# Kernel optimization log

Hardware: AMD Instinct MI355X
Metric: run time of the kernel (lower is better)

## Reference

```python
import jax, jax.numpy as jnp
import numpy as np

N_HEADS = 8
TOP_K = 2
EPS = 1e-5


def cross_node(x4, nf, tkv, Wq, bq, Wk, bk, Wv, bv, Wo, bo, gamma, beta, token_mask):
    # x4: [N, BL, 1, D]; nf: [N, BL, K, D]; tkv: [N, K, 1]; token_mask: [N] float (routed subset)
    N, BL, _, D = x4.shape
    K = nf.shape[2]
    H = N_HEADS
    dh = D // H
    nf = nf * tkv[:, None, :, :]  # use_weights: scale neighbors by topk similarity weights
    xf = x4.reshape(N * BL, D)
    nff = nf.reshape(N * BL, K, D)
    q = (xf @ Wq.T + bq).reshape(N * BL, H, dh)
    k = (nff @ Wk.T + bk).reshape(N * BL, K, H, dh)
    v = (nff @ Wv.T + bv).reshape(N * BL, K, H, dh)
    # flash_attn_func math: scaled dot-product over the K neighbors, per head
    scores = jnp.einsum('thd,tkhd->thk', q, k) / jnp.sqrt(jnp.asarray(dh, xf.dtype))
    attn = jax.nn.softmax(scores, axis=-1)
    o = jnp.einsum('thk,tkhd->thd', attn, v).reshape(N * BL, D)
    o = o @ Wo.T + bo
    # masked BatchNorm1d (training-mode batch stats over ONLY the gathered/routed tokens,
    # matching torch where each expert sees just its subset)
    m = jnp.broadcast_to(token_mask[:, None], (N, BL)).reshape(-1, 1)
    cnt = jnp.maximum(m.sum(), 1.0)
    mean = (o * m).sum(0) / cnt
    var = (((o - mean) ** 2) * m).sum(0) / cnt
    o = (o - mean) / jnp.sqrt(var + EPS) * gamma + beta
    return (o + xf).reshape(N, BL, D)


def moe_forward(x, mm, topk_values, Wr, br, eWq, eWk, eWv, eWo, ebq, ebk, ebv, ebo,
                eGamma, eBeta, eW1, eb1, mWq, mWk, mWv, mWo, mbq, mbk, mbv, mbo,
                mGamma, mBeta, mW2, mb2, topk_indices, modality_index):
    N, B, L, D = x.shape
    BL = B * L
    K = topk_indices.shape[1]
    E = Wr.shape[0]
    Mn = mWq.shape[0]
    # neighbor gather: nf[n, b*l, k] = x[topk_indices[n, k], b, l]
    nf = jnp.transpose(x[topk_indices], (0, 2, 3, 1, 4)).reshape(N, BL, K, D)
    x4 = x.reshape(N, BL, 1, D)
    tkv = topk_values.reshape(N, K, 1)
    # router softmax gating
    gate = jax.nn.softmax(mm.reshape(N, D) @ Wr.T + br, axis=-1)  # [N, E]
    _, te = jax.lax.top_k(gate, TOP_K)
    routed = jax.nn.one_hot(te, E, dtype=gate.dtype).sum(1)  # [N, E] 0/1
    f_i = routed.sum(0) / N
    P_i = gate.sum(0) / N
    balance_loss = E * jnp.sum(f_i * P_i)
    # capacity limiting via running cumsum per expert column
    keep = jnp.cumsum(routed, axis=0) <= (N / E)
    rprobs = gate * jnp.where(keep, routed, jnp.zeros_like(routed))
    active = rprobs.sum(-1) > 0  # [N]
    eprobs, eidx = jax.lax.top_k(rprobs, TOP_K)  # [N, TOP_K]
    # expert dispatch/combine (dense-masked equivalent of the per-expert gather/scatter)
    out_tok = jnp.zeros((N, BL, D), x.dtype)
    for i in range(E):
        sel = (eidx == i).any(-1) & active  # tokens gathered for expert i
        mask_f = sel.astype(x.dtype)
        prob_i = (eprobs * (eidx == i)).sum(-1)  # combine weight (0 for capacity-dropped)
        co = cross_node(x4, nf, tkv, eWq[i], ebq[i], eWk[i], ebk[i], eWv[i], ebv[i],
                        eWo[i], ebo[i], eGamma[i], eBeta[i], mask_f)
        co = co @ eW1[i].T + eb1[i]
        out_tok = out_tok + (mask_f * prob_i)[:, None, None] * co
    # modality experts: every token with modality m goes through modality expert m
    mod_out = jnp.zeros_like(out_tok)
    for m in range(Mn):
        mask_f = (modality_index[:, m, :] == 1).any(-1).astype(x.dtype)
        co = cross_node(x4, nf, tkv, mWq[m], mbq[m], mWk[m], mbk[m], mWv[m], mbv[m],
                        mWo[m], mbo[m], mGamma[m], mBeta[m], mask_f)
        co = co @ mW2[m].T + mb2[m]
        mod_out = mod_out + mask_f[:, None, None] * co
    out = (out_tok + mod_out / Mn).reshape(N, B, L, D)
    return out, balance_loss


def setup_inputs():
    key = jax.random.key(0)
    ks = jax.random.split(key, 7)
    N, B, L, D, K, E, Mn = 1024, 2, 8, 128, 16, 4, 4
    s = 1.0 / float(np.sqrt(D))
    inp = {}
    inp['x'] = jax.random.normal(ks[0], (N, B, L, D), jnp.float32)
    inp['mm'] = jax.random.normal(ks[1], (N, 1, D), jnp.float32)
    inp['topk_values'] = jax.random.uniform(ks[2], (N, K), jnp.float32)
    inp['topk_indices'] = jax.random.randint(ks[3], (N, K), 0, N, dtype=jnp.int32)
    inp['modality_index'] = jax.nn.one_hot(
        jax.random.randint(ks[4], (N,), 0, Mn, dtype=jnp.int32), Mn, dtype=jnp.int32
    ).reshape(N, Mn, 1)
    inp['Wr'] = jax.random.normal(ks[5], (E, D), jnp.float32) * s
    inp['br'] = jnp.zeros((E,), jnp.float32)
    kk = jax.random.split(ks[6], 10)
    for j, nm in enumerate(['eWq', 'eWk', 'eWv', 'eWo', 'eW1']):
        inp[nm] = jax.random.normal(kk[j], (E, D, D), jnp.float32) * s
    for j, nm in enumerate(['mWq', 'mWk', 'mWv', 'mWo', 'mW2']):
        inp[nm] = jax.random.normal(kk[5 + j], (Mn, D, D), jnp.float32) * s
    for nm in ['ebq', 'ebk', 'ebv', 'ebo', 'eBeta', 'eb1']:
        inp[nm] = jnp.zeros((E, D), jnp.float32)
    for nm in ['mbq', 'mbk', 'mbv', 'mbo', 'mBeta', 'mb2']:
        inp[nm] = jnp.zeros((Mn, D), jnp.float32)
    inp['eGamma'] = jnp.ones((E, D), jnp.float32)
    inp['mGamma'] = jnp.ones((Mn, D), jnp.float32)
    return inp


def reference(x, mm, topk_values, topk_indices, modality_index, Wr, br,
              eWq, eWk, eWv, eWo, ebq, ebk, ebv, ebo, eGamma, eBeta, eW1, eb1,
              mWq, mWk, mWv, mWo, mbq, mbk, mbv, mbo, mGamma, mBeta, mW2, mb2):
    return moe_forward(x, mm, topk_values, Wr, br, eWq, eWk, eWv, eWo, ebq, ebk, ebv, ebo,
                       eGamma, eBeta, eW1, eb1, mWq, mWk, mWv, mWo, mbq, mbk, mbv, mbo,
                       mGamma, mBeta, mW2, mb2, topk_indices, modality_index)
```

## Files before the change

### kernel.cpp

```cpp
#include <hip/hip_runtime.h>

typedef unsigned short u16;
typedef unsigned int u32;
typedef short short8 __attribute__((ext_vector_type(8)));
typedef float f32x4 __attribute__((ext_vector_type(4)));

#define NTOK 1024
#define TT 16384
#define DD 128
#define EPSV 1e-5f
#define ST 2097152

__device__ __forceinline__ u16 f2bf(float f) {
    u32 u = __float_as_uint(f);
    u += 0x7fffu + ((u >> 16) & 1u);
    return (u16)(u >> 16);
}
__device__ __forceinline__ u32 pack2(u16 a, u16 b) { return (u32)a | ((u32)b << 16); }
__device__ __forceinline__ void up2(u32 w, float& lo, float& hi) {
    lo = __uint_as_float(w << 16);
    hi = __uint_as_float(w & 0xffff0000u);
}

__global__ __launch_bounds__(256) void k_prep(const float* __restrict__ x,
        const float* __restrict__ eWq, const float* __restrict__ eWk,
        const float* __restrict__ eWv, const float* __restrict__ eWo, const float* __restrict__ eW1,
        const float* __restrict__ mWq, const float* __restrict__ mWk, const float* __restrict__ mWv,
        const float* __restrict__ mWo, const float* __restrict__ mW2,
        const float* __restrict__ mm, const float* __restrict__ Wr, const float* __restrict__ br,
        u16* __restrict__ Xb, u16* __restrict__ Wb, float* __restrict__ logits) {
    int bid = blockIdx.x; int tid = threadIdx.x;
    if (bid < 1024) {
        int i = bid * 256 + tid;
        const float4* p = (const float4*)x + (size_t)i * 2;
        float4 a = p[0], b = p[1];
        uint4 o;
        o.x = pack2(f2bf(a.x), f2bf(a.y));
        o.y = pack2(f2bf(a.z), f2bf(a.w));
        o.z = pack2(f2bf(b.x), f2bf(b.y));
        o.w = pack2(f2bf(b.z), f2bf(b.w));
        *((uint4*)Xb + i) = o;
    } else if (bid < 1344) {
        int i = (bid - 1024) * 256 + tid;
        int tns = i >> 13;
        int off = (i & 8191) * 8;
        const float* src;
        switch (tns) {
            case 0: src = eWq; break; case 1: src = eWk; break; case 2: src = eWv; break;
            case 3: src = eWo; break; case 4: src = eW1; break; case 5: src = mWq; break;
            case 6: src = mWk; break; case 7: src = mWv; break; case 8: src = mWo; break;
            default: src = mW2; break;
        }
        const float4* p = (const float4*)(src + off);
        float4 a = p[0], b = p[1];
        uint4 o;
        o.x = pack2(f2bf(a.x), f2bf(a.y));
        o.y = pack2(f2bf(a.z), f2bf(a.w));
        o.z = pack2(f2bf(b.x), f2bf(b.y));
        o.w = pack2(f2bf(b.z), f2bf(b.w));
        *(uint4*)(Wb + tns * 65536 + off) = o;
    } else {
        int i = (bid - 1344) * 256 + tid;
        int n = i >> 2, e = i & 3;
        const float4* a = (const float4*)(mm + (size_t)n * DD);
        const float4* w = (const float4*)(Wr + (size_t)e * DD);
        float s = 0.f;
#pragma unroll
        for (int j = 0; j < 32; j++) {
            float4 av = a[j], wv = w[j];
            s += av.x * wv.x + av.y * wv.y + av.z * wv.z + av.w * wv.w;
        }
        logits[i] = s + br[e];
    }
}

__global__ __launch_bounds__(1024) void k_route(const float* __restrict__ logits, const int* __restrict__ modix,
                                                float* __restrict__ mask8, float* __restrict__ comb8,
                                                float* __restrict__ cnt8, float* __restrict__ bnsum,
                                                float* __restrict__ bnsq, float* __restrict__ loss) {
    __shared__ int wsum[4][16];
    __shared__ float red[16];
    int n = threadIdx.x;
    if (n < 16) red[n] = 0.f;
    bnsum[n] = 0.f; bnsq[n] = 0.f;
    float g[4];
    float mx = -1e30f;
#pragma unroll
    for (int e = 0; e < 4; e++) { g[e] = logits[n * 4 + e]; mx = fmaxf(mx, g[e]); }
    float s = 0.f;
#pragma unroll
    for (int e = 0; e < 4; e++) { g[e] = expf(g[e] - mx); s += g[e]; }
    float inv = 1.f / s;
#pragma unroll
    for (int e = 0; e < 4; e++) g[e] *= inv;
    int i0 = 0; float b0 = g[0];
#pragma unroll
    for (int e = 1; e < 4; e++) if (g[e] > b0) { b0 = g[e]; i0 = e; }
    int i1 = -1; float b1v = -1e30f;
#pragma unroll
    for (int e = 0; e < 4; e++) if (e != i0 && g[e] > b1v) { b1v = g[e]; i1 = e; }
    u32 rbits = (1u << i0) | (1u << i1);
    int wav = n >> 6, lane = n & 63;
    unsigned long long lm = (~0ull) >> (63 - lane);
    int pre[4];
#pragma unroll
    for (int e = 0; e < 4; e++) {
        unsigned long long m = __ballot((rbits >> e) & 1u);
        pre[e] = __popcll(m & lm);
        if (lane == 63) wsum[e][wav] = __popcll(m);
    }
    __syncthreads();
    float rp[4]; float rsum = 0.f;
#pragma unroll
    for (int e = 0; e < 4; e++) {
        int off = 0;
        for (int w = 0; w < 16; w++) if (w < wav) off += wsum[e][w];
        bool keep = (off + pre[e]) <= 256;
        rp[e] = (((rbits >> e) & 1u) && keep) ? g[e] : 0.f;
        rsum += rp[e];
    }
    bool active = rsum > 0.f;
    int j0 = 0; float c0 = rp[0];
#pragma unroll
    for (int e = 1; e < 4; e++) if (rp[e] > c0) { c0 = rp[e]; j0 = e; }
    int j1 = -1; float c1 = -1e30f;
#pragma unroll
    for (int e = 0; e < 4; e++) if (e != j0 && rp[e] > c1) { c1 = rp[e]; j1 = e; }
    float vals[16];
#pragma unroll
    for (int e = 0; e < 4; e++) {
        bool sel = active && (e == j0 || e == j1);
        float mf = sel ? 1.f : 0.f;
        mask8[e * NTOK + n] = mf;
        comb8[e * NTOK + n] = rp[e];
        vals[e] = mf;
    }
#pragma unroll
    for (int m = 0; m < 4; m++) {
        float mf = (modix[n * 4 + m] == 1) ? 1.f : 0.f;
        mask8[(4 + m) * NTOK + n] = mf;
        comb8[(4 + m) * NTOK + n] = 0.25f * mf;
        vals[4 + m] = mf;
    }
#pragma unroll
    for (int e = 0; e < 4; e++) vals[8 + e] = ((rbits >> e) & 1u) ? 1.f : 0.f;
#pragma unroll
    for (int e = 0; e < 4; e++) vals[12 + e] = g[e];
#pragma unroll
    for (int q = 0; q < 16; q++) {
        float v = vals[q];
        for (int off = 32; off; off >>= 1) v += __shfl_down(v, off, 64);
        if (lane == 0) atomicAdd(&red[q], v);
    }
    __syncthreads();
    if (n == 0) {
        for (int c = 0; c < 8; c++) cnt8[c] = fmaxf(16.f * red[c], 1.f);
        float l = 0.f;
        for (int e = 0; e < 4; e++) l += (red[8 + e] / 1024.f) * (red[12 + e] / 1024.f);
        loss[0] = 4.f * l;
    }
}

__global__ __launch_bounds__(256) void k_gemm_qkv(const u16* __restrict__ Xb, const u16* __restrict__ Wb,
        const float* __restrict__ ebq, const float* __restrict__ mbq,
        const float* __restrict__ mask8,
        u16* __restrict__ Qb, u16* __restrict__ Kb, u16* __restrict__ Vb) {
    __shared__ u16 As[64 * 128];
    __shared__ u16 Bs[128 * 128];
    int tid = threadIdx.x; int bm = blockIdx.x; int c = blockIdx.y;
    int wq = (c < 4) ? c : 20 + (c - 4);
    int wk = (c < 4) ? 4 + c : 24 + (c - 4);
    int wv = (c < 4) ? 8 + c : 28 + (c - 4);
    const u16* Wsl[3] = { Wb + wq * 16384, Wb + wk * 16384, Wb + wv * 16384 };
    const float* bq = (c < 4) ? (ebq + c * 128) : (mbq + (c - 4) * 128);
    u16* Os[3] = { Qb + (size_t)c * ST, Kb + (size_t)c * ST, Vb + (size_t)c * ST };
    const float* maskp = mask8 + c * NTOK;
    bool qact = (maskp[bm * 4] != 0.f) || (maskp[bm * 4 + 1] != 0.f) ||
                (maskp[bm * 4 + 2] != 0.f) || (maskp[bm * 4 + 3] != 0.f);

    const uint4* asrc = (const uint4*)(Xb + (size_t)bm * 8192);
#pragma unroll
    for (int it = 0; it < 4; ++it) {
        int ci = it * 256 + tid;
        uint4 v = asrc[ci];
        int byte = ci * 16; int row = byte >> 8;
        *(uint4*)((char*)As + (byte ^ ((row & 7) << 4))) = v;
    }
    __syncthreads();
    int lane = tid & 63, wid = tid >> 6, lr = lane & 15, lg = lane >> 4;
    short8 a[4];
#pragma unroll
    for (int ks = 0; ks < 4; ++ks) {
        int kk = ks * 64 + lg * 16;
        int arow = wid * 16 + lr;
        a[ks] = *(const short8*)((const char*)As + ((arow * 256 + kk) ^ ((arow & 7) << 4)));
    }
    for (int y = 0; y < 3; ++y) {
        if (y == 0 && !qact) continue;
        const uint4* wsrc = (const uint4*)Wsl[y];
#pragma unroll
        for (int it = 0; it < 8; ++it) {
            int qi = it * 256 + tid;
            uint4 v = wsrc[qi];
            int eo = qi * 8; int row = eo >> 7; int byte = eo * 2;
            *(uint4*)((char*)Bs + (byte ^ ((row & 7) << 4))) = v;
        }
        __syncthreads();
        f32x4 acc[8] = {};
#pragma unroll
        for (int ks = 0; ks < 4; ++ks) {
            int kk = ks * 64 + lg * 16;
#pragma unroll
            for (int nc = 0; nc < 8; ++nc) {
                int brow = nc * 16 + lr;
                short8 b = *(const short8*)((const char*)Bs + ((brow * 256 + kk) ^ ((brow & 7) << 4)));
                acc[nc] = __builtin_amdgcn_mfma_f32_16x16x32_bf16(a[ks], b, acc[nc], 0, 0, 0);
            }
        }
        int row0 = bm * 64 + wid * 16 + lg * 4;
        u16* Op = Os[y];
        bool hasb = (y == 0);
#pragma unroll
        for (int nc = 0; nc < 8; ++nc) {
            int col = nc * 16 + lr;
            float bb = hasb ? bq[col] : 0.f;
#pragma unroll
            for (int r = 0; r < 4; r++)
                Op[(size_t)(row0 + r) * 128 + col] = f2bf(acc[nc][r] + bb);
        }
        __syncthreads();
    }
}

__global__ __launch_bounds__(256) void k_attn(const u16* Qb, const u16* __restrict__ Kb,
        const u16* __restrict__ Vb, const float* __restrict__ tkv, const int* __restrict__ idx,
        const float* __restrict__ ebk, const float* __restrict__ ebv,
        const float* __restrict__ mbk, const float* __restrict__ mbv,
        const float* __restrict__ mask8, u16* Ob) {
    int bid = blockIdx.x;
    int c = bid & 7, inner = bid >> 3;
    int tid = threadIdx.x;
    int gid = inner * 256 + tid;
    int t = gid >> 3, h = gid & 7;
    int n = __builtin_amdgcn_readfirstlane(t >> 4);
    int bl = t & 15;
    if (mask8[c * NTOK + n] == 0.f) return;
    const u16* Qc = Qb + (size_t)c * ST;
    const u16* Kc = Kb + (size_t)c * ST;
    const u16* Vc = Vb + (size_t)c * ST;
    u16* Oc = Ob + (size_t)c * ST;
    const float* bk = (c < 4) ? (ebk + c * 128) : (mbk + (c - 4) * 128);
    const float* bv = (c < 4) ? (ebv + c * 128) : (mbv + (c - 4) * 128);
    float qv[16];
    {
        const uint4* qp = (const uint4*)(Qc + (size_t)t * 128 + h * 16);
        uint4 a = qp[0], b = qp[1];
        up2(a.x, qv[0], qv[1]);   up2(a.y, qv[2], qv[3]);
        up2(a.z, qv[4], qv[5]);   up2(a.w, qv[6], qv[7]);
        up2(b.x, qv[8], qv[9]);   up2(b.y, qv[10], qv[11]);
        up2(b.z, qv[12], qv[13]); up2(b.w, qv[14], qv[15]);
    }
    float qb = 0.f;
#pragma unroll
    for (int i = 0; i < 16; i++) qb += qv[i] * bk[h * 16 + i];
    int gsav[16]; float tsav[16];
#pragma unroll
    for (int k = 0; k < 16; k++) { gsav[k] = idx[n * 16 + k]; tsav[k] = tkv[n * 16 + k]; }
    float scv[16]; float smax = -1e30f;
#pragma unroll 2
    for (int k = 0; k < 16; k++) {
        const uint4* kp = (const uint4*)(Kc + (size_t)(gsav[k] * 16 + bl) * 128 + h * 16);
        uint4 a = kp[0], b = kp[1];
        float d0 = 0.f, d1 = 0.f, lo, hi;
        up2(a.x, lo, hi); d0 = fmaf(lo, qv[0], d0);  d1 = fmaf(hi, qv[1], d1);
        up2(a.y, lo, hi); d0 = fmaf(lo, qv[2], d0);  d1 = fmaf(hi, qv[3], d1);
        up2(a.z, lo, hi); d0 = fmaf(lo, qv[4], d0);  d1 = fmaf(hi, qv[5], d1);
        up2(a.w, lo, hi); d0 = fmaf(lo, qv[6], d0);  d1 = fmaf(hi, qv[7], d1);
        up2(b.x, lo, hi); d0 = fmaf(lo, qv[8], d0);  d1 = fmaf(hi, qv[9], d1);
        up2(b.y, lo, hi); d0 = fmaf(lo, qv[10], d0); d1 = fmaf(hi, qv[11], d1);
        up2(b.z, lo, hi); d0 = fmaf(lo, qv[12], d0); d1 = fmaf(hi, qv[13], d1);
        up2(b.w, lo, hi); d0 = fmaf(lo, qv[14], d0); d1 = fmaf(hi, qv[15], d1);
        float sv = 0.25f * (tsav[k] * (d0 + d1) + qb);
        scv[k] = sv; smax = fmaxf(smax, sv);
    }
    float sum = 0.f;
#pragma unroll
    for (int k = 0; k < 16; k++) { scv[k] = expf(scv[k] - smax); sum += scv[k]; }
    float inv = 1.f / sum;
    float o[16];
#pragma unroll
    for (int i = 0; i < 16; i++) o[i] = 0.f;
#pragma unroll 2
    for (int k = 0; k < 16; k++) {
        const uint4* vp = (const uint4*)(Vc + (size_t)(gsav[k] * 16 + bl) * 128 + h * 16);
        uint4 a = vp[0], b = vp[1];
        float cc = scv[k] * inv * tsav[k];
        float lo, hi;
        up2(a.x, lo, hi); o[0] = fmaf(lo, cc, o[0]);   o[1] = fmaf(hi, cc, o[1]);
        up2(a.y, lo, hi); o[2] = fmaf(lo, cc, o[2]);   o[3] = fmaf(hi, cc, o[3]);
        up2(a.z, lo, hi); o[4] = fmaf(lo, cc, o[4]);   o[5] = fmaf(hi, cc, o[5]);
        up2(a.w, lo, hi); o[6] = fmaf(lo, cc, o[6]);   o[7] = fmaf(hi, cc, o[7]);
        up2(b.x, lo, hi); o[8] = fmaf(lo, cc, o[8]);   o[9] = fmaf(hi, cc, o[9]);
        up2(b.y, lo, hi); o[10] = fmaf(lo, cc, o[10]); o[11] = fmaf(hi, cc, o[11]);
        up2(b.z, lo, hi); o[12] = fmaf(lo, cc, o[12]); o[13] = fmaf(hi, cc, o[13]);
        up2(b.w, lo, hi); o[14] = fmaf(lo, cc, o[14]); o[15] = fmaf(hi, cc, o[15]);
    }
#pragma unroll
    for (int i = 0; i < 16; i++) o[i] += bv[h * 16 + i];
    uint4 s0, s1;
    s0.x = pack2(f2bf(o[0]), f2bf(o[1]));  s0.y = pack2(f2bf(o[2]), f2bf(o[3]));
    s0.z = pack2(f2bf(o[4]), f2bf(o[5]));  s0.w = pack2(f2bf(o[6]), f2bf(o[7]));
    s1.x = pack2(f2bf(o[8]), f2bf(o[9]));  s1.y = pack2(f2bf(o[10]), f2bf(o[11]));
    s1.z = pack2(f2bf(o[12]), f2bf(o[13])); s1.w = pack2(f2bf(o[14]), f2bf(o[15]));
    uint4* op = (uint4*)(Oc + (size_t)t * 128 + h * 16);
    op[0] = s0; op[1] = s1;
}

__global__ __launch_bounds__(256) void k_gemm_o(const u16* __restrict__ Ab, const u16* __restrict__ Wb,
        const float* __restrict__ ebo, const float* __restrict__ mbo,
        u16* __restrict__ O2, const float* __restrict__ mask8,
        float* __restrict__ bnsum, float* __restrict__ bnsq) {
    __shared__ u16 As[64 * 128];
    __shared__ u16 Bs[128 * 128];
    __shared__ float ssum[128], ssq[128];
    int tid = threadIdx.x; int bm = blockIdx.x; int c = blockIdx.y;
    const float* maskp = mask8 + c * NTOK;
    if (maskp[bm * 4] == 0.f && maskp[bm * 4 + 1] == 0.f &&
        maskp[bm * 4 + 2] == 0.f && maskp[bm * 4 + 3] == 0.f) return;
    int wo = (c < 4) ? 12 + c : 32 + (c - 4);
    const u16* Wp = Wb + wo * 16384;
    const float* bo = (c < 4) ? (ebo + c * 128) : (mbo + (c - 4) * 128);
    if (tid < 128) { ssum[tid] = 0.f; ssq[tid] = 0.f; }
    const uint4* asrc = (const uint4*)(Ab + (size_t)c * ST + (size_t)bm * 8192);
#pragma unroll
    for (int it = 0; it < 4; ++it) {
        int ci = it * 256 + tid;
        uint4 v = asrc[ci];
        int byte = ci * 16; int row = byte >> 8;
        *(uint4*)((char*)As + (byte ^ ((row & 7) << 4))) = v;
    }
    const uint4* wsrc = (const uint4*)Wp;
#pragma unroll
    for (int it = 0; it < 8; ++it) {
        int qi = it * 256 + tid;
        uint4 v = wsrc[qi];
        int eo = qi * 8; int row = eo >> 7; int byte = eo * 2;
        *(uint4*)((char*)Bs + (byte ^ ((row & 7) << 4))) = v;
    }
    __syncthreads();
    int lane = tid & 63, wid = tid >> 6, lr = lane & 15, lg = lane >> 4;
    f32x4 acc[8] = {};
#pragma unroll
    for (int ks = 0; ks < 4; ++ks) {
        int kk = ks * 64 + lg * 16;
        int arow = wid * 16 + lr;
        short8 a = *(const short8*)((const char*)As + ((arow * 256 + kk) ^ ((arow & 7) << 4)));
#pragma unroll
        for (int nc = 0; nc < 8; ++nc) {
            int brow = nc * 16 + lr;
            short8 b = *(const short8*)((const char*)Bs + ((brow * 256 + kk) ^ ((brow & 7) << 4)));
            acc[nc] = __builtin_amdgcn_mfma_f32_16x16x32_bf16(a, b, acc[nc], 0, 0, 0);
        }
    }
    int nidx = bm * 4 + wid;
    float mk = maskp[nidx];
    int row0 = bm * 64 + wid * 16 + lg * 4;
    u16* O2c = O2 + (size_t)c * ST;
    float ps[8], pq[8];
#pragma unroll
    for (int nc = 0; nc < 8; ++nc) {
        int col = nc * 16 + lr;
        float bb = bo[col];
        float sv = 0.f, qv = 0.f;
#pragma unroll
        for (int r = 0; r < 4; r++) {
            float v = acc[nc][r] + bb;
            if (mk != 0.f) O2c[(size_t)(row0 + r) * 128 + col] = f2bf(v);
            sv += v; qv += v * v;
        }
        ps[nc] = sv * mk; pq[nc] = qv * mk;
    }
#pragma unroll
    for (int nc = 0; nc < 8; ++nc) {
        ps[nc] += __shfl_xor(ps[nc], 16, 64); ps[nc] += __shfl_xor(ps[nc], 32, 64);
        pq[nc] += __shfl_xor(pq[nc], 16, 64); pq[nc] += __shfl_xor(pq[nc], 32, 64);
    }
    if (lane < 16) {
#pragma unroll
        for (int nc = 0; nc < 8; ++nc) {
            atomicAdd(&ssum[nc * 16 + lane], ps[nc]);
            atomicAdd(&ssq[nc * 16 + lane], pq[nc]);
        }
    }
    __syncthreads();
    if (tid < 128) { atomicAdd(&bnsum[c * 128 + tid], ssum[tid]); atomicAdd(&bnsq[c * 128 + tid], ssq[tid]); }
}

__global__ __launch_bounds__(512) void k_gemm_w1(const u16* __restrict__ O2, const u16* __restrict__ Xb,
        const u16* __restrict__ Wb, const float* __restrict__ eb1, const float* __restrict__ mb2,
        const float* __restrict__ eGamma, const float* __restrict__ mGamma,
        const float* __restrict__ eBeta, const float* __restrict__ mBeta,
        const float* __restrict__ comb8, const float* __restrict__ cnt8,
        const float* __restrict__ bnsum, const float* __restrict__ bnsq,
        float* __restrict__ out) {
    __shared__ u16 As[64 * 128];
    __shared__ u16 Bs[128 * 128];
    __shared__ float scall[8][128], shall[8][128];
    int tid = threadIdx.x; int bm = blockIdx.x;
#pragma unroll
    for (int j = 0; j < 2; ++j) {
        int id = j * 512 + tid;
        int c = id >> 7, d = id & 127;
        float cnt = cnt8[c];
        float mean = bnsum[c * 128 + d] / cnt;
        float var = bnsq[c * 128 + d] / cnt - mean * mean;
        float rs = rsqrtf(var + EPSV);
        const float* ga = (c < 4) ? (eGamma + c * 128) : (mGamma + (c - 4) * 128);
        const float* be = (c < 4) ? (eBeta + c * 128) : (mBeta + (c - 4) * 128);
        float gg = ga[d];
        scall[c][d] = rs * gg;
        shall[c][d] = be[d] - mean * rs * gg;
    }
    __syncthreads();
    int lane = tid & 63, wid = tid >> 6, lr = lane & 15, lg = lane >> 4;
    int wm = wid & 3, wn = wid >> 2;
    f32x4 acc[4] = {};
    const uint4* xsrc = (const uint4*)(Xb + (size_t)bm * 8192);
    for (int c = 0; c < 8; ++c) {
        float wc4[4];
        wc4[0] = comb8[c * NTOK + bm * 4];     wc4[1] = comb8[c * NTOK + bm * 4 + 1];
        wc4[2] = comb8[c * NTOK + bm * 4 + 2]; wc4[3] = comb8[c * NTOK + bm * 4 + 3];
        if (wc4[0] == 0.f && wc4[1] == 0.f && wc4[2] == 0.f && wc4[3] == 0.f) continue;
        int wsl = (c < 4) ? 16 + c : 36 + (c - 4);
        const u16* Wp = Wb + wsl * 16384;
        const uint4* osrc = (const uint4*)(O2 + (size_t)c * ST + (size_t)bm * 8192);
#pragma unroll
        for (int it = 0; it < 2; ++it) {
            int qi = it * 512 + tid;
            int eo = qi * 8; int row = eo >> 7; int cb = eo & 127;
            float wc = wc4[row >> 4];
            uint4 ov = osrc[qi]; uint4 xv = xsrc[qi];
            float olo, ohi, xlo, xhi;
            uint4 hh;
            up2(ov.x, olo, ohi); up2(xv.x, xlo, xhi);
            hh.x = pack2(f2bf((olo * scall[c][cb] + shall[c][cb] + xlo) * wc),
                         f2bf((ohi * scall[c][cb + 1] + shall[c][cb + 1] + xhi) * wc));
            up2(ov.y, olo, ohi); up2(xv.y, xlo, xhi);
            hh.y = pack2(f2bf((olo * scall[c][cb + 2] + shall[c][cb + 2] + xlo) * wc),
                         f2bf((ohi * scall[c][cb + 3] + shall[c][cb + 3] + xhi) * wc));
            up2(ov.z, olo, ohi); up2(xv.z, xlo, xhi);
            hh.z = pack2(f2bf((olo * scall[c][cb + 4] + shall[c][cb + 4] + xlo) * wc),
                         f2bf((ohi * scall[c][cb + 5] + shall[c][cb + 5] + xhi) * wc));
            up2(ov.w, olo, ohi); up2(xv.w, xlo, xhi);
            hh.w = pack2(f2bf((olo * scall[c][cb + 6] + shall[c][cb + 6] + xlo) * wc),
                         f2bf((ohi * scall[c][cb + 7] + shall[c][cb + 7] + xhi) * wc));
            *(uint4*)((char*)As + ((eo * 2) ^ ((row & 7) << 4))) = hh;
        }
        const uint4* wsrc = (const uint4*)Wp;
#pragma unroll
        for (int it = 0; it < 4; ++it) {
            int qi = it * 512 + tid;
            uint4 v = wsrc[qi];
            int eo = qi * 8; int row = eo >> 7; int byte = eo * 2;
            *(uint4*)((char*)Bs + (byte ^ ((row & 7) << 4))) = v;
        }
        __syncthreads();
#pragma unroll
        for (int ks = 0; ks < 4; ++ks) {
            int kk = ks * 64 + lg * 16;
            int arow = wm * 16 + lr;
            short8 a = *(const short8*)((const char*)As + ((arow * 256 + kk) ^ ((arow & 7) << 4)));
#pragma unroll
            for (int nc = 0; nc < 4; ++nc) {
                int brow = wn * 64 + nc * 16 + lr;
                short8 b = *(const short8*)((const char*)Bs + ((brow * 256 + kk) ^ ((brow & 7) << 4)));
                acc[nc] = __builtin_amdgcn_mfma_f32_16x16x32_bf16(a, b, acc[nc], 0, 0, 0);
            }
        }
        __syncthreads();
    }
    int nidx = bm * 4 + wm;
    int row0 = bm * 64 + wm * 16 + lg * 4;
    float wc8[8];
#pragma unroll
    for (int c = 0; c < 8; ++c) wc8[c] = comb8[c * NTOK + nidx];
#pragma unroll
    for (int nc = 0; nc < 4; ++nc) {
        int col = wn * 64 + nc * 16 + lr;
        float bias = 0.f;
#pragma unroll
        for (int c = 0; c < 8; ++c) {
            const float* b1 = (c < 4) ? (eb1 + c * 128) : (mb2 + (c - 4) * 128);
            bias += wc8[c] * b1[col];
        }
#pragma unroll
        for (int r = 0; r < 4; r++)
            out[(size_t)(row0 + r) * 128 + col] = acc[nc][r] + bias;
    }
}

extern "C" void kernel_launch(void* const* d_in, const int* in_sizes, int n_in,
                              void* d_out, int out_size, void* d_ws, size_t ws_size,
                              hipStream_t stream) {
    (void)in_sizes; (void)n_in; (void)ws_size; (void)out_size;
    const float* x    = (const float*)d_in[0];
    const float* mm   = (const float*)d_in[1];
    const float* tkv  = (const float*)d_in[2];
    const int*   idx  = (const int*)d_in[3];
    const int*   modi = (const int*)d_in[4];
    const float* Wr   = (const float*)d_in[5];
    const float* br   = (const float*)d_in[6];
    const float* eWq = (const float*)d_in[7],  *eWk = (const float*)d_in[8],  *eWv = (const float*)d_in[9];
    const float* eWo = (const float*)d_in[10], *eW1 = (const float*)d_in[11];
    const float* mWq = (const float*)d_in[12], *mWk = (const float*)d_in[13], *mWv = (const float*)d_in[14];
    const float* mWo = (const float*)d_in[15], *mW2 = (const float*)d_in[16];
    const float* ebq = (const float*)d_in[17], *ebk = (const float*)d_in[18], *ebv = (const float*)d_in[19];
    const float* ebo = (const float*)d_in[20], *eBeta = (const float*)d_in[21], *eb1 = (const float*)d_in[22];
    const float* mbq = (const float*)d_in[23], *mbk = (const float*)d_in[24], *mbv = (const float*)d_in[25];
    const float* mbo = (const float*)d_in[26], *mBeta = (const float*)d_in[27], *mb2 = (const float*)d_in[28];
    const float* eGamma = (const float*)d_in[29], *mGamma = (const float*)d_in[30];
    float* out = (float*)d_out;

    char* wsb = (char*)d_ws;
    const size_t MB = 1024 * 1024;
    u16* Xb = (u16*)wsb;
    u16* Wb = (u16*)(wsb + 4 * MB);
    u16* Qb = (u16*)(wsb + 8 * MB);
    u16* Kb = (u16*)(wsb + 40 * MB);
    u16* Vb = (u16*)(wsb + 72 * MB);
    u16* O2 = (u16*)(wsb + 104 * MB);
    float* logits = (float*)(wsb + 136 * MB);
    float* comb8 = logits + 4096;
    float* mask8 = comb8 + 8192;
    float* cnt8  = mask8 + 8192;
    float* bnsum = cnt8 + 16;
    float* bnsq  = bnsum + 1024;

    k_prep<<<1360, 256, 0, stream>>>(x, eWq, eWk, eWv, eWo, eW1, mWq, mWk, mWv, mWo, mW2,
                                     mm, Wr, br, Xb, Wb, logits);
    k_route<<<1, 1024, 0, stream>>>(logits, modi, mask8, comb8, cnt8, bnsum, bnsq,
                                    out + (size_t)TT * DD);
    k_gemm_qkv<<<dim3(256, 8), 256, 0, stream>>>(Xb, Wb, ebq, mbq, mask8, Qb, Kb, Vb);
    k_attn<<<4096, 256, 0, stream>>>(Qb, Kb, Vb, tkv, idx, ebk, ebv, mbk, mbv, mask8, Qb);
    k_gemm_o<<<dim3(256, 8), 256, 0, stream>>>(Qb, Wb, ebo, mbo, O2, mask8, bnsum, bnsq);
    k_gemm_w1<<<256, 512, 0, stream>>>(O2, Xb, Wb, eb1, mb2, eGamma, mGamma, eBeta, mBeta,
                                       comb8, cnt8, bnsum, bnsq, out);
}
```

Measured before the change: 119.0 us.

## Fuse neighbor attention into output-projection GEMM via shared-memory A tile

```diff
diff --git a/kernel.cpp b/kernel.cpp
--- a/kernel.cpp
+++ b/kernel.cpp
@@ -20,6 +20,9 @@
 __device__ __forceinline__ void up2(u32 w, float& lo, float& hi) {
     lo = __uint_as_float(w << 16);
     hi = __uint_as_float(w & 0xffff0000u);
+}
+__device__ __forceinline__ float rfl_f(float v) {
+    return __uint_as_float(__builtin_amdgcn_readfirstlane(__float_as_uint(v)));
 }
 
 __global__ __launch_bounds__(256) void k_prep(const float* __restrict__ x,
@@ -232,144 +235,146 @@
     }
 }
 
-__global__ __launch_bounds__(256) void k_attn(const u16* Qb, const u16* __restrict__ Kb,
+__global__ __launch_bounds__(512) void k_attn_o(const u16* __restrict__ Qb, const u16* __restrict__ Kb,
         const u16* __restrict__ Vb, const float* __restrict__ tkv, const int* __restrict__ idx,
         const float* __restrict__ ebk, const float* __restrict__ ebv,
         const float* __restrict__ mbk, const float* __restrict__ mbv,
-        const float* __restrict__ mask8, u16* Ob) {
-    int bid = blockIdx.x;
-    int c = bid & 7, inner = bid >> 3;
-    int tid = threadIdx.x;
-    int gid = inner * 256 + tid;
-    int t = gid >> 3, h = gid & 7;
-    int n = __builtin_amdgcn_readfirstlane(t >> 4);
-    int bl = t & 15;
-    if (mask8[c * NTOK + n] == 0.f) return;
-    const u16* Qc = Qb + (size_t)c * ST;
-    const u16* Kc = Kb + (size_t)c * ST;
-    const u16* Vc = Vb + (size_t)c * ST;
-    u16* Oc = Ob + (size_t)c * ST;
-    const float* bk = (c < 4) ? (ebk + c * 128) : (mbk + (c - 4) * 128);
-    const float* bv = (c < 4) ? (ebv + c * 128) : (mbv + (c - 4) * 128);
-    float qv[16];
-    {
-        const uint4* qp = (const uint4*)(Qc + (size_t)t * 128 + h * 16);
-        uint4 a = qp[0], b = qp[1];
-        up2(a.x, qv[0], qv[1]);   up2(a.y, qv[2], qv[3]);
-        up2(a.z, qv[4], qv[5]);   up2(a.w, qv[6], qv[7]);
-        up2(b.x, qv[8], qv[9]);   up2(b.y, qv[10], qv[11]);
-        up2(b.z, qv[12], qv[13]); up2(b.w, qv[14], qv[15]);
-    }
-    float qb = 0.f;
-#pragma unroll
-    for (int i = 0; i < 16; i++) qb += qv[i] * bk[h * 16 + i];
-    int gsav[16]; float tsav[16];
-#pragma unroll
-    for (int k = 0; k < 16; k++) { gsav[k] = idx[n * 16 + k]; tsav[k] = tkv[n * 16 + k]; }
-    float scv[16]; float smax = -1e30f;
-#pragma unroll 2
-    for (int k = 0; k < 16; k++) {
-        const uint4* kp = (const uint4*)(Kc + (size_t)(gsav[k] * 16 + bl) * 128 + h * 16);
-        uint4 a = kp[0], b = kp[1];
-        float d0 = 0.f, d1 = 0.f, lo, hi;
-        up2(a.x, lo, hi); d0 = fmaf(lo, qv[0], d0);  d1 = fmaf(hi, qv[1], d1);
-        up2(a.y, lo, hi); d0 = fmaf(lo, qv[2], d0);  d1 = fmaf(hi, qv[3], d1);
-        up2(a.z, lo, hi); d0 = fmaf(lo, qv[4], d0);  d1 = fmaf(hi, qv[5], d1);
-        up2(a.w, lo, hi); d0 = fmaf(lo, qv[6], d0);  d1 = fmaf(hi, qv[7], d1);
-        up2(b.x, lo, hi); d0 = fmaf(lo, qv[8], d0);  d1 = fmaf(hi, qv[9], d1);
-        up2(b.y, lo, hi); d0 = fmaf(lo, qv[10], d0); d1 = fmaf(hi, qv[11], d1);
-        up2(b.z, lo, hi); d0 = fmaf(lo, qv[12], d0); d1 = fmaf(hi, qv[13], d1);
-        up2(b.w, lo, hi); d0 = fmaf(lo, qv[14], d0); d1 = fmaf(hi, qv[15], d1);
-        float sv = 0.25f * (tsav[k] * (d0 + d1) + qb);
-        scv[k] = sv; smax = fmaxf(smax, sv);
-    }
-    float sum = 0.f;
-#pragma unroll
-    for (int k = 0; k < 16; k++) { scv[k] = expf(scv[k] - smax); sum += scv[k]; }
-    float inv = 1.f / sum;
-    float o[16];
-#pragma unroll
-    for (int i = 0; i < 16; i++) o[i] = 0.f;
-#pragma unroll 2
-    for (int k = 0; k < 16; k++) {
-        const uint4* vp = (const uint4*)(Vc + (size_t)(gsav[k] * 16 + bl) * 128 + h * 16);
-        uint4 a = vp[0], b = vp[1];
-        float cc = scv[k] * inv * tsav[k];
-        float lo, hi;
-        up2(a.x, lo, hi); o[0] = fmaf(lo, cc, o[0]);   o[1] = fmaf(hi, cc, o[1]);
-        up2(a.y, lo, hi); o[2] = fmaf(lo, cc, o[2]);   o[3] = fmaf(hi, cc, o[3]);
-        up2(a.z, lo, hi); o[4] = fmaf(lo, cc, o[4]);   o[5] = fmaf(hi, cc, o[5]);
-        up2(a.w, lo, hi); o[6] = fmaf(lo, cc, o[6]);   o[7] = fmaf(hi, cc, o[7]);
-        up2(b.x, lo, hi); o[8] = fmaf(lo, cc, o[8]);   o[9] = fmaf(hi, cc, o[9]);
-        up2(b.y, lo, hi); o[10] = fmaf(lo, cc, o[10]); o[11] = fmaf(hi, cc, o[11]);
-        up2(b.z, lo, hi); o[12] = fmaf(lo, cc, o[12]); o[13] = fmaf(hi, cc, o[13]);
-        up2(b.w, lo, hi); o[14] = fmaf(lo, cc, o[14]); o[15] = fmaf(hi, cc, o[15]);
-    }
-#pragma unroll
-    for (int i = 0; i < 16; i++) o[i] += bv[h * 16 + i];
-    uint4 s0, s1;
-    s0.x = pack2(f2bf(o[0]), f2bf(o[1]));  s0.y = pack2(f2bf(o[2]), f2bf(o[3]));
-    s0.z = pack2(f2bf(o[4]), f2bf(o[5]));  s0.w = pack2(f2bf(o[6]), f2bf(o[7]));
-    s1.x = pack2(f2bf(o[8]), f2bf(o[9]));  s1.y = pack2(f2bf(o[10]), f2bf(o[11]));
-    s1.z = pack2(f2bf(o[12]), f2bf(o[13])); s1.w = pack2(f2bf(o[14]), f2bf(o[15]));
-    uint4* op = (uint4*)(Oc + (size_t)t * 128 + h * 16);
-    op[0] = s0; op[1] = s1;
-}
-
-__global__ __launch_bounds__(256) void k_gemm_o(const u16* __restrict__ Ab, const u16* __restrict__ Wb,
-        const float* __restrict__ ebo, const float* __restrict__ mbo,
-        u16* __restrict__ O2, const float* __restrict__ mask8,
+        const u16* __restrict__ Wb, const float* __restrict__ ebo, const float* __restrict__ mbo,
+        const float* __restrict__ mask8, u16* __restrict__ O2,
         float* __restrict__ bnsum, float* __restrict__ bnsq) {
     __shared__ u16 As[64 * 128];
     __shared__ u16 Bs[128 * 128];
     __shared__ float ssum[128], ssq[128];
-    int tid = threadIdx.x; int bm = blockIdx.x; int c = blockIdx.y;
+    int bid = blockIdx.x;
+    int c = bid & 7, bm = bid >> 3;
     const float* maskp = mask8 + c * NTOK;
-    if (maskp[bm * 4] == 0.f && maskp[bm * 4 + 1] == 0.f &&
-        maskp[bm * 4 + 2] == 0.f && maskp[bm * 4 + 3] == 0.f) return;
+    float m4[4];
+    m4[0] = maskp[bm * 4];     m4[1] = maskp[bm * 4 + 1];
+    m4[2] = maskp[bm * 4 + 2]; m4[3] = maskp[bm * 4 + 3];
+    if (m4[0] == 0.f && m4[1] == 0.f && m4[2] == 0.f && m4[3] == 0.f) return;
+    int tid = threadIdx.x;
+    if (tid < 128) { ssum[tid] = 0.f; ssq[tid] = 0.f; }
     int wo = (c < 4) ? 12 + c : 32 + (c - 4);
-    const u16* Wp = Wb + wo * 16384;
-    const float* bo = (c < 4) ? (ebo + c * 128) : (mbo + (c - 4) * 128);
-    if (tid < 128) { ssum[tid] = 0.f; ssq[tid] = 0.f; }
-    const uint4* asrc = (const uint4*)(Ab + (size_t)c * ST + (size_t)bm * 8192);
+    const uint4* wsrc = (const uint4*)(Wb + wo * 16384);
+    uint4 bst[4];
+#pragma unroll
+    for (int it = 0; it < 4; ++it) bst[it] = wsrc[it * 512 + tid];
+
+    int tl = tid >> 3, h = tid & 7;
+    int nl = tl >> 4;
+    int n = bm * 4 + nl;
+    float mk_n = m4[nl];
+    int b0 = tl * 256 + h * 32;
+    int sw = (tl & 7) << 4;
+    if (mk_n != 0.f) {
+        const u16* Qc = Qb + (size_t)c * ST;
+        const u16* Kc = Kb + (size_t)c * ST;
+        const u16* Vc = Vb + (size_t)c * ST;
+        const float* bk = (c < 4) ? (ebk + c * 128) : (mbk + (c - 4) * 128);
+        const float* bv = (c < 4) ? (ebv + c * 128) : (mbv + (c - 4) * 128);
+        int t = bm * 64 + tl;
+        int bl = tl & 15;
+        float qv[16];
+        {
+            const uint4* qp = (const uint4*)(Qc + (size_t)t * 128 + h * 16);
+            uint4 a = qp[0], b = qp[1];
+            up2(a.x, qv[0], qv[1]);   up2(a.y, qv[2], qv[3]);
+            up2(a.z, qv[4], qv[5]);   up2(a.w, qv[6], qv[7]);
+            up2(b.x, qv[8], qv[9]);   up2(b.y, qv[10], qv[11]);
+            up2(b.z, qv[12], qv[13]); up2(b.w, qv[14], qv[15]);
+        }
+        float qb = 0.f;
+#pragma unroll
+        for (int i = 0; i < 16; i++) qb += qv[i] * bk[h * 16 + i];
+        int gsav[16]; float tsav[16];
+#pragma unroll
+        for (int k = 0; k < 16; k++) {
+            gsav[k] = __builtin_amdgcn_readfirstlane(idx[n * 16 + k]);
+            tsav[k] = rfl_f(tkv[n * 16 + k]);
+        }
+        float scv[16]; float smax = -1e30f;
+#pragma unroll 2
+        for (int k = 0; k < 16; k++) {
+            const uint4* kp = (const uint4*)(Kc + (size_t)(gsav[k] * 16 + bl) * 128 + h * 16);
+            uint4 a = kp[0], b = kp[1];
+            float d0 = 0.f, d1 = 0.f, lo, hi;
+            up2(a.x, lo, hi); d0 = fmaf(lo, qv[0], d0);  d1 = fmaf(hi, qv[1], d1);
+            up2(a.y, lo, hi); d0 = fmaf(lo, qv[2], d0);  d1 = fmaf(hi, qv[3], d1);
+            up2(a.z, lo, hi); d0 = fmaf(lo, qv[4], d0);  d1 = fmaf(hi, qv[5], d1);
+            up2(a.w, lo, hi); d0 = fmaf(lo, qv[6], d0);  d1 = fmaf(hi, qv[7], d1);
+            up2(b.x, lo, hi); d0 = fmaf(lo, qv[8], d0);  d1 = fmaf(hi, qv[9], d1);
+            up2(b.y, lo, hi); d0 = fmaf(lo, qv[10], d0); d1 = fmaf(hi, qv[11], d1);
+            up2(b.z, lo, hi); d0 = fmaf(lo, qv[12], d0); d1 = fmaf(hi, qv[13], d1);
+            up2(b.w, lo, hi); d0 = fmaf(lo, qv[14], d0); d1 = fmaf(hi, qv[15], d1);
+            float sv = 0.25f * (tsav[k] * (d0 + d1) + qb);
+            scv[k] = sv; smax = fmaxf(smax, sv);
+        }
+        float sum = 0.f;
+#pragma unroll
+        for (int k = 0; k < 16; k++) { scv[k] = __expf(scv[k] - smax); sum += scv[k]; }
+        float inv = 1.f / sum;
+        float o[16];
+#pragma unroll
+        for (int i = 0; i < 16; i++) o[i] = 0.f;
+#pragma unroll 2
+        for (int k = 0; k < 16; k++) {
+            const uint4* vp = (const uint4*)(Vc + (size_t)(gsav[k] * 16 + bl) * 128 + h * 16);
+            uint4 a = vp[0], b = vp[1];
+            float cc = scv[k] * inv * tsav[k];
+            float lo, hi;
+            up2(a.x, lo, hi); o[0] = fmaf(lo, cc, o[0]);   o[1] = fmaf(hi, cc, o[1]);
+            up2(a.y, lo, hi); o[2] = fmaf(lo, cc, o[2]);   o[3] = fmaf(hi, cc, o[3]);
+            up2(a.z, lo, hi); o[4] = fmaf(lo, cc, o[4]);   o[5] = fmaf(hi, cc, o[5]);
+            up2(a.w, lo, hi); o[6] = fmaf(lo, cc, o[6]);   o[7] = fmaf(hi, cc, o[7]);
+            up2(b.x, lo, hi); o[8] = fmaf(lo, cc, o[8]);   o[9] = fmaf(hi, cc, o[9]);
+            up2(b.y, lo, hi); o[10] = fmaf(lo, cc, o[10]); o[11] = fmaf(hi, cc, o[11]);
+            up2(b.z, lo, hi); o[12] = fmaf(lo, cc, o[12]); o[13] = fmaf(hi, cc, o[13]);
+            up2(b.w, lo, hi); o[14] = fmaf(lo, cc, o[14]); o[15] = fmaf(hi, cc, o[15]);
+        }
+#pragma unroll
+        for (int i = 0; i < 16; i++) o[i] += bv[h * 16 + i];
+        uint4 s0, s1;
+        s0.x = pack2(f2bf(o[0]), f2bf(o[1]));  s0.y = pack2(f2bf(o[2]), f2bf(o[3]));
+        s0.z = pack2(f2bf(o[4]), f2bf(o[5]));  s0.w = pack2(f2bf(o[6]), f2bf(o[7]));
+        s1.x = pack2(f2bf(o[8]), f2bf(o[9]));  s1.y = pack2(f2bf(o[10]), f2bf(o[11]));
+        s1.z = pack2(f2bf(o[12]), f2bf(o[13])); s1.w = pack2(f2bf(o[14]), f2bf(o[15]));
+        *(uint4*)((char*)As + (b0 ^ sw)) = s0;
+        *(uint4*)((char*)As + ((b0 + 16) ^ sw)) = s1;
+    } else {
+        uint4 z = {0u, 0u, 0u, 0u};
+        *(uint4*)((char*)As + (b0 ^ sw)) = z;
+        *(uint4*)((char*)As + ((b0 + 16) ^ sw)) = z;
+    }
 #pragma unroll
     for (int it = 0; it < 4; ++it) {
-        int ci = it * 256 + tid;
-        uint4 v = asrc[ci];
-        int byte = ci * 16; int row = byte >> 8;
-        *(uint4*)((char*)As + (byte ^ ((row & 7) << 4))) = v;
-    }
-    const uint4* wsrc = (const uint4*)Wp;
-#pragma unroll
-    for (int it = 0; it < 8; ++it) {
-        int qi = it * 256 + tid;
-        uint4 v = wsrc[qi];
+        int qi = it * 512 + tid;
         int eo = qi * 8; int row = eo >> 7; int byte = eo * 2;
-        *(uint4*)((char*)Bs + (byte ^ ((row & 7) << 4))) = v;
+        *(uint4*)((char*)Bs + (byte ^ ((row & 7) << 4))) = bst[it];
     }
     __syncthreads();
     int lane = tid & 63, wid = tid >> 6, lr = lane & 15, lg = lane >> 4;
-    f32x4 acc[8] = {};
+    int wm = wid & 3, wn = wid >> 2;
+    f32x4 acc[4] = {};
 #pragma unroll
     for (int ks = 0; ks < 4; ++ks) {
         int kk = ks * 64 + lg * 16;
-        int arow = wid * 16 + lr;
+        int arow = wm * 16 + lr;
         short8 a = *(const short8*)((const char*)As + ((arow * 256 + kk) ^ ((arow & 7) << 4)));
 #pragma unroll
-        for (int nc = 0; nc < 8; ++nc) {
-            int brow = nc * 16 + lr;
+        for (int nc = 0; nc < 4; ++nc) {
+            int brow = wn * 64 + nc * 16 + lr;
             short8 b = *(const short8*)((const char*)Bs + ((brow * 256 + kk) ^ ((brow & 7) << 4)));
             acc[nc] = __builtin_amdgcn_mfma_f32_16x16x32_bf16(a, b, acc[nc], 0, 0, 0);
         }
     }
-    int nidx = bm * 4 + wid;
-    float mk = maskp[nidx];
-    int row0 = bm * 64 + wid * 16 + lg * 4;
+    const float* bo = (c < 4) ? (ebo + c * 128) : (mbo + (c - 4) * 128);
+    float mk = m4[wm];
+    int row0 = bm * 64 + wm * 16 + lg * 4;
     u16* O2c = O2 + (size_t)c * ST;
-    float ps[8], pq[8];
-#pragma unroll
-    for (int nc = 0; nc < 8; ++nc) {
-        int col = nc * 16 + lr;
+    float ps[4], pq[4];
+#pragma unroll
+    for (int nc = 0; nc < 4; ++nc) {
+        int col = wn * 64 + nc * 16 + lr;
         float bb = bo[col];
         float sv = 0.f, qv = 0.f;
 #pragma unroll
@@ -381,15 +386,15 @@
         ps[nc] = sv * mk; pq[nc] = qv * mk;
     }
 #pragma unroll
-    for (int nc = 0; nc < 8; ++nc) {
+    for (int nc = 0; nc < 4; ++nc) {
         ps[nc] += __shfl_xor(ps[nc], 16, 64); ps[nc] += __shfl_xor(ps[nc], 32, 64);
         pq[nc] += __shfl_xor(pq[nc], 16, 64); pq[nc] += __shfl_xor(pq[nc], 32, 64);
     }
     if (lane < 16) {
 #pragma unroll
-        for (int nc = 0; nc < 8; ++nc) {
-            atomicAdd(&ssum[nc * 16 + lane], ps[nc]);
-            atomicAdd(&ssq[nc * 16 + lane], pq[nc]);
+        for (int nc = 0; nc < 4; ++nc) {
+            atomicAdd(&ssum[wn * 64 + nc * 16 + lane], ps[nc]);
+            atomicAdd(&ssq[wn * 64 + nc * 16 + lane], pq[nc]);
         }
     }
     __syncthreads();
@@ -541,8 +546,8 @@
     k_route<<<1, 1024, 0, stream>>>(logits, modi, mask8, comb8, cnt8, bnsum, bnsq,
                                     out + (size_t)TT * DD);
     k_gemm_qkv<<<dim3(256, 8), 256, 0, stream>>>(Xb, Wb, ebq, mbq, mask8, Qb, Kb, Vb);
-    k_attn<<<4096, 256, 0, stream>>>(Qb, Kb, Vb, tkv, idx, ebk, ebv, mbk, mbv, mask8, Qb);
-    k_gemm_o<<<dim3(256, 8), 256, 0, stream>>>(Qb, Wb, ebo, mbo, O2, mask8, bnsum, bnsq);
+    k_attn_o<<<2048, 512, 0, stream>>>(Qb, Kb, Vb, tkv, idx, ebk, ebv, mbk, mbv,
+                                       Wb, ebo, mbo, mask8, O2, bnsum, bnsq);
     k_gemm_w1<<<256, 512, 0, stream>>>(O2, Xb, Wb, eb1, mb2, eGamma, mGamma, eBeta, mBeta,
                                        comb8, cnt8, bnsum, bnsq, out);
 }
```

Measured after the change: 133.0 us. +11.7%, slower.
